# Kernel tuning notes

Measured on AMD Instinct MI355X. Metric: run time of the kernel, lower is better.

Reference implementation:

```python
import jax, jax.numpy as jnp
import numpy as np


def _ln(x, w, b, eps=1e-5):
    m = x.mean(-1, keepdims=True)
    v = ((x - m) ** 2).mean(-1, keepdims=True)
    return (x - m) * jax.lax.rsqrt(v + eps) * w + b


def _selective_scan(u, delta, A, Bm, Cm, D):
    # u, delta: (G, Dd, L); A: (G, Dd, N); Bm, Cm: (G, N, L); D: (G, Dd)
    G, Dd, L = u.shape
    N = A.shape[-1]

    def step(h, t):
        dt, ut, bt, ct = t  # (G,Dd), (G,Dd), (G,N), (G,N)
        h = jnp.exp(dt[..., None] * A) * h + (dt * ut)[..., None] * bt[:, None, :]
        return h, jnp.einsum('gdn,gn->gd', h, ct)

    h0 = jnp.zeros((G, Dd, N), u.dtype)
    xs_t = (jnp.moveaxis(delta, -1, 0), jnp.moveaxis(u, -1, 0),
            jnp.moveaxis(Bm, -1, 0), jnp.moveaxis(Cm, -1, 0))
    _, ys = jax.lax.scan(step, h0, xs_t)  # ys: (L, G, Dd)
    return jnp.moveaxis(ys, 0, -1) + D[..., None] * u


def _forward_core(xc, x_proj_w, dt_proj_w, dt_proj_b, A_log, Ds):
    # xc: (B, Di, H, W) -> SS2D 4-direction cross-scan selective scan
    B, Di, H, W = xc.shape
    L = H * W
    K, Ctot, _ = x_proj_w.shape
    N = A_log.shape[-1]
    R = Ctot - 2 * N
    x_hw = xc.reshape(B, Di, L)
    x_wh = xc.transpose(0, 1, 3, 2).reshape(B, Di, L)
    xs = jnp.stack([x_hw, x_wh, x_hw[:, :, ::-1], x_wh[:, :, ::-1]], axis=1)  # (B,K,Di,L)
    x_dbl = jnp.einsum('bkdl,kcd->bkcl', xs, x_proj_w)
    dtr, Bm, Cm = x_dbl[:, :, :R], x_dbl[:, :, R:R + N], x_dbl[:, :, R + N:]
    dts = jax.nn.softplus(jnp.einsum('bkrl,kdr->bkdl', dtr, dt_proj_w)
                          + dt_proj_b[None, :, :, None])
    A = -jnp.exp(A_log)  # (K, Di, N)
    G = B * K
    ys = _selective_scan(
        xs.reshape(G, Di, L), dts.reshape(G, Di, L),
        jnp.broadcast_to(A, (B, K, Di, N)).reshape(G, Di, N),
        Bm.reshape(G, N, L), Cm.reshape(G, N, L),
        jnp.broadcast_to(Ds, (B, K, Di)).reshape(G, Di),
    ).reshape(B, K, Di, L)
    inv_wh = lambda t: t.reshape(B, Di, W, H).transpose(0, 1, 3, 2).reshape(B, Di, L)
    y = ys[:, 0] + inv_wh(ys[:, 1]) + ys[:, 2, :, ::-1] + inv_wh(ys[:, 3, :, ::-1])
    return y.reshape(B, Di, H, W).transpose(0, 2, 3, 1)  # (B, H, W, Di)


def _vss_block(xh, ln_w, ln_b, in_w, cw, cb, xp, dtw, dtb, Alog, Dsk, onw, onb, ow):
    # xh: (B, H, W, C); residual VSS block with SS2D
    Di = cw.shape[0]
    h = _ln(xh, ln_w, ln_b)
    xz = h @ in_w.T  # (B,H,W,2*Di)
    xc, z = xz[..., :Di], xz[..., Di:]
    xc = xc.transpose(0, 3, 1, 2)  # (B,Di,H,W)
    xc = jax.lax.conv_general_dilated(
        xc, cw[:, None], (1, 1), 'SAME',
        feature_group_count=Di, dimension_numbers=('NCHW', 'OIHW', 'NCHW')
    ) + cb[None, :, None, None]
    xc = jax.nn.silu(xc)
    y = _forward_core(xc, xp, dtw, dtb, Alog, Dsk)
    y = _ln(y, onw, onb) * jax.nn.silu(z)
    return xh + y @ ow.T


def _fwd(x, skip, pe_expand_w, pe_norm_w, pe_norm_b, lp_w, lp_b,
         blk_ln_w, blk_ln_b, in_proj_w, conv_w, conv_b, x_proj_w,
         dt_proj_w, dt_proj_b, A_log, Ds, out_norm_w, out_norm_b, out_proj_w):
    B, Cin, H, W = x.shape
    c = Cin // 2
    xh = x.transpose(0, 2, 3, 1) @ pe_expand_w.T  # (B,H,W,2*Cin)
    xh = xh.reshape(B, H, W, 2, 2, c).transpose(0, 1, 3, 2, 4, 5).reshape(B, 2 * H, 2 * W, c)
    xh = _ln(xh, pe_norm_w, pe_norm_b)
    # concat with skip along channels, then per-pixel linear projection
    xh = jnp.concatenate([xh, skip.transpose(0, 2, 3, 1)], axis=-1)
    xh = xh @ lp_w.T + lp_b
    for i in range(blk_ln_w.shape[0]):
        xh = _vss_block(xh, blk_ln_w[i], blk_ln_b[i], in_proj_w[i], conv_w[i], conv_b[i],
                        x_proj_w[i], dt_proj_w[i], dt_proj_b[i], A_log[i], Ds[i],
                        out_norm_w[i], out_norm_b[i], out_proj_w[i])
    return xh.transpose(0, 3, 1, 2)  # (B, out_dim, 2H, 2W)


def setup_inputs():
    key = jax.random.key(0)
    ks = jax.random.split(key, 10)
    B, H, W = 2, 16, 16
    in_dim, skip_dim, out_dim, depth = 768, 384, 384, 2
    Di, N, R, K = 2 * out_dim, 16, out_dim // 16, 4
    s = 0.02
    return {
        'x': jax.random.normal(ks[0], (B, in_dim, H, W), jnp.float32),
        'skip': jax.random.normal(ks[1], (B, skip_dim, 2 * H, 2 * W), jnp.float32),
        'pe_expand_w': jax.random.normal(ks[2], (2 * in_dim, in_dim)) * s,
        'pe_norm_w': jnp.ones((in_dim // 2,)),
        'pe_norm_b': jnp.zeros((in_dim // 2,)),
        'lp_w': jax.random.normal(ks[3], (out_dim, skip_dim + in_dim // 2)) * s,
        'lp_b': jnp.zeros((out_dim,)),
        'blk_ln_w': jnp.ones((depth, out_dim)),
        'blk_ln_b': jnp.zeros((depth, out_dim)),
        'in_proj_w': jax.random.normal(ks[4], (depth, 2 * Di, out_dim)) * s,
        'conv_w': jax.random.normal(ks[5], (depth, Di, 3, 3)) * s,
        'conv_b': jnp.zeros((depth, Di)),
        'x_proj_w': jax.random.normal(ks[6], (depth, K, R + 2 * N, Di)) * s,
        'dt_proj_w': jax.random.normal(ks[7], (depth, K, Di, R)) * s,
        'dt_proj_b': jax.random.normal(ks[8], (depth, K, Di)) * s,
        'A_log': jnp.log(jnp.broadcast_to(jnp.arange(1, N + 1, dtype=jnp.float32), (depth, K, Di, N)) + 0.0),
        'Ds': jnp.ones((depth, K, Di)),
        'out_norm_w': jnp.ones((depth, Di)),
        'out_norm_b': jnp.zeros((depth, Di)),
        'out_proj_w': jax.random.normal(ks[9], (depth, out_dim, Di)) * s,
    }


def reference(x, skip, pe_expand_w, pe_norm_w, pe_norm_b, lp_w, lp_b,
              blk_ln_w, blk_ln_b, in_proj_w, conv_w, conv_b, x_proj_w,
              dt_proj_w, dt_proj_b, A_log, Ds, out_norm_w, out_norm_b, out_proj_w):
    return _fwd(x, skip, pe_expand_w, pe_norm_w, pe_norm_b, lp_w, lp_b,
                blk_ln_w, blk_ln_b, in_proj_w, conv_w, conv_b, x_proj_w,
                dt_proj_w, dt_proj_b, A_log, Ds, out_norm_w, out_norm_b, out_proj_w)
```

## Files before the change

### kernel.cpp

```cpp
#include <hip/hip_runtime.h>
#include <math.h>


typedef __attribute__((ext_vector_type(8))) short s8v;
typedef __attribute__((ext_vector_type(4))) float f4v;

static __device__ __forceinline__ float sigmoidf_(float x) {
    return 1.f / (1.f + __expf(-x));
}
static __device__ __forceinline__ ushort f2bf(float x) {
    unsigned u = __float_as_uint(x);
    return (ushort)((u + 0x7fff + ((u >> 16) & 1)) >> 16);
}
static __device__ __forceinline__ float bf2f(ushort u) {
    return __uint_as_float(((unsigned)u) << 16);
}

static __device__ __forceinline__ int scan_pos(int k, int l) {
    int m = (k & 2) ? (1023 - l) : l;
    return (k & 1) ? (((m & 31) << 5) | (m >> 5)) : m;
}

__global__ __launch_bounds__(256) void cvt_all_k(
    const float* __restrict__ pew, const float* __restrict__ lpw,
    const float* __restrict__ inw, const float* __restrict__ ow,
    const float* __restrict__ xpw, const float* __restrict__ dtw,
    ushort* __restrict__ wpe, ushort* __restrict__ wlp,
    ushort* __restrict__ winb, ushort* __restrict__ wob,
    ushort* __restrict__ wxpp, ushort* __restrict__ wdtp) {
    int g = blockIdx.x * 256 + threadIdx.x;
    if (g < 811008) {
        const float* s; ushort* d; int off;
        if (g < 294912)      { s = pew;  d = wpe;  off = g; }
        else if (g < 368640) { s = lpw;  d = wlp;  off = g - 294912; }
        else if (g < 663552) { s = inw;  d = winb; off = g - 368640; }
        else                 { s = ow;   d = wob;  off = g - 663552; }
        float4 v = ((const float4*)s)[off];
        ushort4 o = {f2bf(v.x), f2bf(v.y), f2bf(v.z), f2bf(v.w)};
        ((ushort4*)d)[off] = o;
    } else if (g < 909312) {
        int e = g - 811008;
        int blkb = e / 49152, rem = e % 49152;
        int n = rem / 192, q = rem % 192;
        int k = n >> 6, c = n & 63;
        ushort4 o = {0, 0, 0, 0};
        if (c < 56) {
            float4 v = *(const float4*)(xpw +
                ((size_t)((blkb * 4 + k) * 56 + c)) * 768 + q * 4);
            o = {f2bf(v.x), f2bf(v.y), f2bf(v.z), f2bf(v.w)};
        }
        ((ushort4*)wxpp)[e] = o;
    } else {
        int e = g - 909312;
        int rowk = e >> 3, q = e & 7;
        ushort4 o = {0, 0, 0, 0};
        if (q < 6) {
            float4 v = *(const float4*)(dtw + (size_t)rowk * 24 + q * 4);
            o = {f2bf(v.x), f2bf(v.y), f2bf(v.z), f2bf(v.w)};
        }
        ((ushort4*)wdtp)[e] = o;
    }
}

__global__ __launch_bounds__(256) void tr_x_k(const float* __restrict__ x,
                                              ushort* __restrict__ o) {
    __shared__ float tile[32][33];
    int b = blockIdx.z, c0 = blockIdx.y * 32, s0 = blockIdx.x * 32;
    int tx = threadIdx.x & 31, ty = threadIdx.x >> 5;
    for (int i = ty; i < 32; i += 8)
        tile[i][tx] = x[((size_t)(b * 768 + c0 + i)) * 256 + s0 + tx];
    __syncthreads();
    for (int i = ty; i < 32; i += 8)
        o[((size_t)(b * 256 + s0 + i)) * 768 + c0 + tx] = f2bf(tile[tx][i]);
}

__global__ __launch_bounds__(256) void peskip_k(const float* __restrict__ t1,
                                                const float* __restrict__ pnw,
                                                const float* __restrict__ pnb,
                                                const float* __restrict__ skip,
                                                ushort* __restrict__ cin) {
    __shared__ float tile[32][33];
    int bx = blockIdx.x;
    if (bx < 512) {
        int w = threadIdx.x >> 6, lane = threadIdx.x & 63;
        int row = bx * 4 + w;
        int b = row >> 10, p = row & 1023;
        int r = p >> 5, col = p & 31;
        int i = r >> 1, a = r & 1, j = col >> 1, b2 = col & 1;
        const float* src =
            t1 + ((size_t)(b * 256 + i * 16 + j)) * 1536 + (a * 2 + b2) * 384;
        float v[6], s1 = 0.f, s2 = 0.f;
#pragma unroll
        for (int q = 0; q < 6; ++q) {
            v[q] = src[lane + 64 * q];
            s1 += v[q]; s2 += v[q] * v[q];
        }
#pragma unroll
        for (int m = 1; m < 64; m <<= 1) {
            s1 += __shfl_xor(s1, m); s2 += __shfl_xor(s2, m);
        }
        float mean = s1 * (1.f / 384.f);
        float rstd = rsqrtf(s2 * (1.f / 384.f) - mean * mean + 1e-5f);
        ushort* o = cin + (size_t)row * 768;
#pragma unroll
        for (int q = 0; q < 6; ++q) {
            int c = lane + 64 * q;
            o[c] = f2bf((v[q] - mean) * rstd * pnw[c] + pnb[c]);
        }
    } else {
        int idx = bx - 512;
        int b = idx / 384, rem = idx % 384;
        int c0 = (rem / 32) * 32, s0 = (rem % 32) * 32;
        int tx = threadIdx.x & 31, ty = threadIdx.x >> 5;
        for (int i = ty; i < 32; i += 8)
            tile[i][tx] = skip[((size_t)(b * 384 + c0 + i)) * 1024 + s0 + tx];
        __syncthreads();
        for (int i = ty; i < 32; i += 8)
            cin[((size_t)(b * 1024 + s0 + i)) * 768 + 384 + c0 + tx] =
                f2bf(tile[tx][i]);
    }
}

__global__ __launch_bounds__(256) void tr_out_k(const float* __restrict__ xh,
                                                float* __restrict__ out) {
    __shared__ float tile[32][33];
    int b = blockIdx.z, p0 = blockIdx.x * 32, c0 = blockIdx.y * 32;
    int tx = threadIdx.x & 31, ty = threadIdx.x >> 5;
    for (int i = ty; i < 32; i += 8)
        tile[i][tx] = xh[((size_t)(b * 1024 + p0 + i)) * 384 + c0 + tx];
    __syncthreads();
    for (int i = ty; i < 32; i += 8)
        out[((size_t)(b * 384 + c0 + i)) * 1024 + p0 + tx] = tile[tx][i];
}

template <int BN>
__global__ __launch_bounds__(256) void gemm_t(const ushort* __restrict__ A,
                                              const ushort* __restrict__ B,
                                              const float* __restrict__ bias,
                                              const float* __restrict__ res,
                                              float* __restrict__ Cf,
                                              ushort* __restrict__ Cb,
                                              float* __restrict__ dblBC,
                                              ushort* __restrict__ dtrb,
                                              int M, int N, int K,
                                              long sAz, long sBz, long sBiz,
                                              long sCz, int mode) {
    constexpr int MI = (BN == 128) ? 4 : 2;
    __shared__ ushort Als[2][128][40];
    __shared__ ushort Bls[2][BN][40];
    A += (size_t)blockIdx.z * sAz;
    B += (size_t)blockIdx.z * sBz;
    if (Cf) Cf += (size_t)blockIdx.z * sCz;
    if (Cb) Cb += (size_t)blockIdx.z * sCz;
    if (bias) bias += (size_t)blockIdx.z * sBiz;
    int t = threadIdx.x;
    int bm = blockIdx.y * 128, bn = blockIdx.x * BN;
    int lane = t & 63, w = t >> 6;
    int wm = (BN == 128) ? (w & 1) * 64 : w * 32;
    int wn = (BN == 128) ? (w >> 1) * 64 : 0;
    int r16 = lane & 15, quad = lane >> 4;
    int srow = t >> 1, shalf = t & 1;
    int brow = (BN == 128) ? (t >> 1) : (t >> 2);
    int bq   = (BN == 128) ? (t & 1) * 16 : (t & 3) * 8;
    f4v acc[MI][4] = {};
    const ushort* Ag = A + (size_t)(bm + srow) * K + shalf * 16;
    const ushort* Bg = B + (size_t)(bn + brow) * K + bq;
    int nt = K >> 5;
    uint4 a0, a1, b0, b1;
    a0 = *(const uint4*)(Ag);
    a1 = *(const uint4*)(Ag + 8);
    b0 = *(const uint4*)(Bg);
    if (BN == 128) b1 = *(const uint4*)(Bg + 8);
    *(uint4*)&Als[0][srow][shalf * 16] = a0;
    *(uint4*)&Als[0][srow][shalf * 16 + 8] = a1;
    *(uint4*)&Bls[0][brow][bq] = b0;
    if (BN == 128) *(uint4*)&Bls[0][brow][bq + 8] = b1;
    for (int it = 0; it < nt; ++it) {
        int buf = it & 1;
        __syncthreads();
        if (it + 1 < nt) {
            int k0 = (it + 1) << 5;
            a0 = *(const uint4*)(Ag + k0);
            a1 = *(const uint4*)(Ag + k0 + 8);
            b0 = *(const uint4*)(Bg + k0);
            if (BN == 128) b1 = *(const uint4*)(Bg + k0 + 8);
        }
        s8v af[MI], bfr[4];
#pragma unroll
        for (int i = 0; i < MI; ++i)
            af[i] = *(const s8v*)&Als[buf][wm + i * 16 + r16][quad * 8];
#pragma unroll
        for (int j = 0; j < 4; ++j)
            bfr[j] = *(const s8v*)&Bls[buf][wn + j * 16 + r16][quad * 8];
#pragma unroll
        for (int i = 0; i < MI; ++i)
#pragma unroll
            for (int j = 0; j < 4; ++j)
                acc[i][j] = __builtin_amdgcn_mfma_f32_16x16x32_bf16(
                    af[i], bfr[j], acc[i][j], 0, 0, 0);
        if (it + 1 < nt) {
            *(uint4*)&Als[buf ^ 1][srow][shalf * 16] = a0;
            *(uint4*)&Als[buf ^ 1][srow][shalf * 16 + 8] = a1;
            *(uint4*)&Bls[buf ^ 1][brow][bq] = b0;
            if (BN == 128) *(uint4*)&Bls[buf ^ 1][brow][bq + 8] = b1;
        }
    }
#pragma unroll
    for (int i = 0; i < MI; ++i) {
        int row0 = bm + wm + i * 16 + quad * 4;
#pragma unroll
        for (int j = 0; j < 4; ++j) {
            int col = bn + wn + j * 16 + r16;
            float bv = bias ? bias[col] : 0.f;
#pragma unroll
            for (int r = 0; r < 4; ++r) {
                int row = row0 + r;
                float v = acc[i][j][r] + bv;
                if (mode == 0) {
                    if (res) v += res[(size_t)row * N + col];
                    Cf[(size_t)row * N + col] = v;
                } else if (mode == 1) {
                    v = (v > 20.f) ? v : __logf(1.f + __expf(v));
                    Cb[(size_t)row * N + col] = f2bf(v);
                } else {
                    int k = col >> 6, c = col & 63;
                    int b = row >> 10, p = row & 1023;
                    if (c < 32)
                        dtrb[((size_t)k * 2048 + row) * 32 + c] =
                            f2bf((c < 24) ? v : 0.f);
                    if (c >= 24 && c < 56) {
                        int l = scan_pos(k, p);
                        dblBC[(((size_t)(b * 4 + k)) * 1024 + l) * 32 + (c - 24)] = v;
                    }
                }
            }
        }
    }
}

__global__ __launch_bounds__(256) void dt_perm_k(const ushort* __restrict__ dtsp,
                                                 ushort* __restrict__ dtscan) {
    int r = blockIdx.x * 2 + (threadIdx.x >> 7);
    int t = threadIdx.x & 127;
    int l = r & 1023;
    int kb2 = r >> 10;
    int k = kb2 >> 1, b = kb2 & 1;
    int p = scan_pos(k, l);
    const uint* s = (const uint*)(dtsp + ((size_t)(k * 2048 + b * 1024 + p)) * 768);
    uint* d = (uint*)(dtscan + (size_t)r * 768);
    d[t] = s[t];
    d[t + 128] = s[t + 128];
    d[t + 256] = s[t + 256];
}

__global__ __launch_bounds__(256) void ln_rows_384(const float* __restrict__ in,
                                                   const float* __restrict__ wgt,
                                                   const float* __restrict__ bb,
                                                   ushort* __restrict__ out) {
    int w = threadIdx.x >> 6, lane = threadIdx.x & 63;
    int row = blockIdx.x * 4 + w;
    const float* x = in + (size_t)row * 384;
    float v[6], s1 = 0.f, s2 = 0.f;
#pragma unroll
    for (int q = 0; q < 6; ++q) {
        v[q] = x[lane + 64 * q];
        s1 += v[q]; s2 += v[q] * v[q];
    }
#pragma unroll
    for (int m = 1; m < 64; m <<= 1) {
        s1 += __shfl_xor(s1, m); s2 += __shfl_xor(s2, m);
    }
    float mean = s1 * (1.f / 384.f);
    float rstd = rsqrtf(s2 * (1.f / 384.f) - mean * mean + 1e-5f);
#pragma unroll
    for (int q = 0; q < 6; ++q) {
        int c = lane + 64 * q;
        out[(size_t)row * 384 + c] = f2bf((v[q] - mean) * rstd * wgt[c] + bb[c]);
    }
}

__global__ __launch_bounds__(256) void conv_silu_k(const float* __restrict__ xz,
                                                   const float* __restrict__ cw,
                                                   const float* __restrict__ cb,
                                                   ushort* __restrict__ xcb,
                                                   ushort* __restrict__ xcwh) {
    int row = blockIdx.x;
    int b = row >> 10, p = row & 1023;
    int r = p >> 5, col = p & 31;
    int mwh = ((p & 31) << 5) | (p >> 5);
    for (int d = threadIdx.x; d < 768; d += 256) {
        float acc = cb[d];
#pragma unroll
        for (int dy = 0; dy < 3; ++dy) {
            int rr = r + dy - 1;
            if ((unsigned)rr > 31u) continue;
#pragma unroll
            for (int dx = 0; dx < 3; ++dx) {
                int cc = col + dx - 1;
                if ((unsigned)cc > 31u) continue;
                acc += cw[d * 9 + dy * 3 + dx] *
                       xz[((size_t)(b * 1024 + rr * 32 + cc)) * 1536 + d];
            }
        }
        float o = acc * sigmoidf_(acc);
        ushort ob = f2bf(o);
        xcb[(size_t)row * 768 + d] = ob;
        xcwh[((size_t)(b * 1024 + mwh)) * 768 + d] = ob;
    }
}


__global__ __launch_bounds__(64) void scan_p1(const ushort* __restrict__ dtscan,
                                              const float* __restrict__ dblBC,
                                              const ushort* __restrict__ xcb,
                                              const ushort* __restrict__ xcwh,
                                              const float* __restrict__ alog,
                                              float* __restrict__ Pg,
                                              float* __restrict__ Hg) {
    __shared__ float sB[32][16];
    int lane = threadIdx.x;
    int d0 = blockIdx.x * 64, ch = blockIdx.y, kb = blockIdx.z;
    int k = kb & 3, b = kb >> 2;
    int d = d0 + lane;
    float A2[16];
    {
        const float4* ap = (const float4*)(alog + ((size_t)(k * 768 + d)) * 16);
#pragma unroll
        for (int q = 0; q < 4; ++q) {
            float4 v = ap[q];
            A2[4 * q + 0] = -__expf(v.x) * 1.44269504f;
            A2[4 * q + 1] = -__expf(v.y) * 1.44269504f;
            A2[4 * q + 2] = -__expf(v.z) * 1.44269504f;
            A2[4 * q + 3] = -__expf(v.w) * 1.44269504f;
        }
    }
    int l0 = ch * 32;
    const ushort* dts = dtscan + ((size_t)((k * 2 + b) * 1024 + l0)) * 768 + d;
    const ushort* ub = ((k & 1) ? xcwh : xcb) + (size_t)b * 786432 + d;
    const float* bcp = dblBC + (size_t)kb * 1024 * 32;
    float rdt[32], ru[32], rB[8];
#pragma unroll
    for (int i = 0; i < 32; ++i) rdt[i] = bf2f(dts[(size_t)i * 768]);
    if (k & 2) {
#pragma unroll
        for (int i = 0; i < 32; ++i)
            ru[i] = bf2f(ub[(size_t)(1023 - (l0 + i)) * 768]);
    } else {
#pragma unroll
        for (int i = 0; i < 32; ++i) ru[i] = bf2f(ub[(size_t)(l0 + i) * 768]);
    }
    int bi = lane >> 4, bn_ = lane & 15;
#pragma unroll
    for (int j = 0; j < 8; ++j)
        rB[j] = bcp[(size_t)(l0 + bi + 4 * j) * 32 + bn_];
#pragma unroll
    for (int j = 0; j < 8; ++j) sB[bi + 4 * j][bn_] = rB[j];
    __syncthreads();
    float h[16], P[16];
#pragma unroll
    for (int n = 0; n < 16; ++n) { h[n] = 0.f; P[n] = 1.f; }
#pragma unroll 4
    for (int i = 0; i < 32; ++i) {
        float dtv = rdt[i], dtu = dtv * ru[i];
        const float4* B4 = (const float4*)&sB[i][0];
        float4 q0 = B4[0], q1 = B4[1], q2 = B4[2], q3 = B4[3];
        float Bv[16] = {q0.x, q0.y, q0.z, q0.w, q1.x, q1.y, q1.z, q1.w,
                        q2.x, q2.y, q2.z, q2.w, q3.x, q3.y, q3.z, q3.w};
#pragma unroll
        for (int n = 0; n < 16; ++n) {
            float a = __builtin_amdgcn_exp2f(dtv * A2[n]);
            P[n] *= a;
            h[n] = a * h[n] + dtu * Bv[n];
        }
    }
    float* pp = Pg + ((size_t)(kb * 32 + ch)) * 12288 + d * 16;
    float* hp = Hg + ((size_t)(kb * 32 + ch)) * 12288 + d * 16;
#pragma unroll
    for (int q = 0; q < 4; ++q) {
        float4 pv = {P[4 * q], P[4 * q + 1], P[4 * q + 2], P[4 * q + 3]};
        float4 hv = {h[4 * q], h[4 * q + 1], h[4 * q + 2], h[4 * q + 3]};
        *(float4*)(pp + 4 * q) = pv;
        *(float4*)(hp + 4 * q) = hv;
    }
}

__global__ __launch_bounds__(256) void comb_k(const float* __restrict__ Pg,
                                              const float* __restrict__ Hg,
                                              float* __restrict__ H0g) {
    int t = blockIdx.x * 256 + threadIdx.x;
    int kb = t / 12288, dn = t % 12288;
    size_t base = (size_t)kb * 32 * 12288 + dn;
    float pv[31], hv[31];
#pragma unroll
    for (int ch = 0; ch < 31; ++ch) {
        pv[ch] = Pg[base + (size_t)ch * 12288];
        hv[ch] = Hg[base + (size_t)ch * 12288];
    }
    float h = 0.f;
    H0g[base] = 0.f;
#pragma unroll
    for (int ch = 0; ch < 31; ++ch) {
        h = pv[ch] * h + hv[ch];
        H0g[base + (size_t)(ch + 1) * 12288] = h;
    }
}

__global__ __launch_bounds__(64) void scan_p2(const ushort* __restrict__ dtscan,
                                              const float* __restrict__ dblBC,
                                              const ushort* __restrict__ xcb,
                                              const ushort* __restrict__ xcwh,
                                              const float* __restrict__ alog,
                                              const float* __restrict__ H0g,
                                              ushort* __restrict__ y4b) {
    __shared__ float sB[32][16];
    __shared__ float sC[32][16];
    int lane = threadIdx.x;
    int d0 = blockIdx.x * 64, ch = blockIdx.y, kb = blockIdx.z;
    int k = kb & 3, b = kb >> 2;
    int d = d0 + lane;
    float A2[16];
    {
        const float4* ap = (const float4*)(alog + ((size_t)(k * 768 + d)) * 16);
#pragma unroll
        for (int q = 0; q < 4; ++q) {
            float4 v = ap[q];
            A2[4 * q + 0] = -__expf(v.x) * 1.44269504f;
            A2[4 * q + 1] = -__expf(v.y) * 1.44269504f;
            A2[4 * q + 2] = -__expf(v.z) * 1.44269504f;
            A2[4 * q + 3] = -__expf(v.w) * 1.44269504f;
        }
    }
    float h[16];
    {
        const float4* h0p =
            (const float4*)(H0g + ((size_t)(kb * 32 + ch)) * 12288 + d * 16);
#pragma unroll
        for (int q = 0; q < 4; ++q) {
            float4 hv = h0p[q];
            h[4 * q + 0] = hv.x; h[4 * q + 1] = hv.y;
            h[4 * q + 2] = hv.z; h[4 * q + 3] = hv.w;
        }
    }
    int l0 = ch * 32;
    const ushort* dts = dtscan + ((size_t)((k * 2 + b) * 1024 + l0)) * 768 + d;
    const ushort* ub = ((k & 1) ? xcwh : xcb) + (size_t)b * 786432 + d;
    const float* bcp = dblBC + (size_t)kb * 1024 * 32;
    ushort* yp = y4b + ((size_t)(kb * 1024 + l0)) * 768 + d;
    float rdt[32], ru[32], rB[8], rC[8];
#pragma unroll
    for (int i = 0; i < 32; ++i) rdt[i] = bf2f(dts[(size_t)i * 768]);
    if (k & 2) {
#pragma unroll
        for (int i = 0; i < 32; ++i)
            ru[i] = bf2f(ub[(size_t)(1023 - (l0 + i)) * 768]);
    } else {
#pragma unroll
        for (int i = 0; i < 32; ++i) ru[i] = bf2f(ub[(size_t)(l0 + i) * 768]);
    }
    int bi = lane >> 4, bn_ = lane & 15;
#pragma unroll
    for (int j = 0; j < 8; ++j) {
        rB[j] = bcp[(size_t)(l0 + bi + 4 * j) * 32 + bn_];
        rC[j] = bcp[(size_t)(l0 + bi + 4 * j) * 32 + 16 + bn_];
    }
#pragma unroll
    for (int j = 0; j < 8; ++j) {
        sB[bi + 4 * j][bn_] = rB[j];
        sC[bi + 4 * j][bn_] = rC[j];
    }
    __syncthreads();
#pragma unroll 4
    for (int i = 0; i < 32; ++i) {
        float dtv = rdt[i], dtu = dtv * ru[i];
        const float4* B4 = (const float4*)&sB[i][0];
        const float4* C4 = (const float4*)&sC[i][0];
        float4 q0 = B4[0], q1 = B4[1], q2 = B4[2], q3 = B4[3];
        float Bv[16] = {q0.x, q0.y, q0.z, q0.w, q1.x, q1.y, q1.z, q1.w,
                        q2.x, q2.y, q2.z, q2.w, q3.x, q3.y, q3.z, q3.w};
        float4 c0 = C4[0], c1 = C4[1], c2 = C4[2], c3 = C4[3];
        float Cv[16] = {c0.x, c0.y, c0.z, c0.w, c1.x, c1.y, c1.z, c1.w,
                        c2.x, c2.y, c2.z, c2.w, c3.x, c3.y, c3.z, c3.w};
        float y = 0.f;
#pragma unroll
        for (int n = 0; n < 16; ++n) {
            float a = __builtin_amdgcn_exp2f(dtv * A2[n]);
            h[n] = a * h[n] + dtu * Bv[n];
            y += h[n] * Cv[n];
        }
        yp[(size_t)i * 768] = f2bf(y);
    }
}

__global__ __launch_bounds__(256) void fuse_out_k(const ushort* __restrict__ y4b,
                                                  const ushort* __restrict__ xcb,
                                                  const float* __restrict__ xz,
                                                  const float* __restrict__ ds,
                                                  const float* __restrict__ onw,
                                                  const float* __restrict__ onb,
                                                  ushort* __restrict__ g) {
    int w = threadIdx.x >> 6, lane = threadIdx.x & 63;
    int row = blockIdx.x * 4 + w;
    int b = row >> 10, p = row & 1023;
    int l0 = scan_pos(0, p), l1 = scan_pos(1, p);
    int l2 = scan_pos(2, p), l3 = scan_pos(3, p);
    const ushort* y0 = y4b + ((size_t)((b * 4 + 0) * 1024 + l0)) * 768;
    const ushort* y1 = y4b + ((size_t)((b * 4 + 1) * 1024 + l1)) * 768;
    const ushort* y2 = y4b + ((size_t)((b * 4 + 2) * 1024 + l2)) * 768;
    const ushort* y3 = y4b + ((size_t)((b * 4 + 3) * 1024 + l3)) * 768;
    float v[12], s1 = 0.f, s2 = 0.f;
#pragma unroll
    for (int q = 0; q < 12; ++q) {
        int d = lane + 64 * q;
        float u = bf2f(xcb[(size_t)row * 768 + d]);
        float dsum = ds[d] + ds[768 + d] + ds[1536 + d] + ds[2304 + d];
        float val = dsum * u + bf2f(y0[d]) + bf2f(y1[d]) + bf2f(y2[d]) + bf2f(y3[d]);
        v[q] = val; s1 += val; s2 += val * val;
    }
#pragma unroll
    for (int m = 1; m < 64; m <<= 1) {
        s1 += __shfl_xor(s1, m); s2 += __shfl_xor(s2, m);
    }
    float mean = s1 * (1.f / 768.f);
    float rstd = rsqrtf(s2 * (1.f / 768.f) - mean * mean + 1e-5f);
#pragma unroll
    for (int q = 0; q < 12; ++q) {
        int d = lane + 64 * q;
        float zz = xz[(size_t)row * 1536 + 768 + d];
        float sil = zz * sigmoidf_(zz);
        g[(size_t)row * 768 + d] = f2bf(((v[q] - mean) * rstd * onw[d] + onb[d]) * sil);
    }
}

extern "C" void kernel_launch(void* const* d_in, const int* in_sizes, int n_in,
                              void* d_out, int out_size, void* d_ws, size_t ws_size,
                              hipStream_t stream) {
    const float* x    = (const float*)d_in[0];
    const float* skip = (const float*)d_in[1];
    const float* pew  = (const float*)d_in[2];
    const float* pnw  = (const float*)d_in[3];
    const float* pnb  = (const float*)d_in[4];
    const float* lpw  = (const float*)d_in[5];
    const float* lpb  = (const float*)d_in[6];
    const float* blw  = (const float*)d_in[7];
    const float* blb  = (const float*)d_in[8];
    const float* inw  = (const float*)d_in[9];
    const float* cw   = (const float*)d_in[10];
    const float* cb   = (const float*)d_in[11];
    const float* xpw  = (const float*)d_in[12];
    const float* dtw  = (const float*)d_in[13];
    const float* dtbi = (const float*)d_in[14];
    const float* alog = (const float*)d_in[15];
    const float* ds   = (const float*)d_in[16];
    const float* onw  = (const float*)d_in[17];
    const float* onb  = (const float*)d_in[18];
    const float* ow   = (const float*)d_in[19];
    float* out = (float*)d_out;

    char* base = (char*)d_ws;
    auto alloc = [&](size_t bytes) -> char* {
        char* p = base;
        base += (bytes + 255) & ~(size_t)255;
        return p;
    };
    float*  xh    = (float*)alloc(2048 * 384 * 4);
    ushort* hbuf  = (ushort*)alloc(2048 * 768 * 2);
    float*  xz    = (float*)alloc((size_t)2048 * 1536 * 4);
    ushort* xcb   = (ushort*)alloc(2048 * 768 * 2);
    ushort* xcwh  = (ushort*)alloc(2048 * 768 * 2);
    float*  dblBC = (float*)alloc(8192 * 32 * 4);
    ushort* dtrb  = (ushort*)alloc((size_t)4 * 2048 * 32 * 2);
    ushort* dtsp  = (ushort*)alloc((size_t)4 * 2048 * 768 * 2);
    ushort* dtscan= (ushort*)alloc((size_t)4 * 2048 * 768 * 2);
    ushort* y4b   = (ushort*)alloc((size_t)8192 * 768 * 2);
    float*  Pg    = (float*)alloc((size_t)8 * 32 * 12288 * 4);
    float*  Hg    = (float*)alloc((size_t)8 * 32 * 12288 * 4);
    float*  H0g   = (float*)alloc((size_t)8 * 32 * 12288 * 4);
    ushort* xspe  = (ushort*)alloc(512 * 768 * 2);
    float*  t1    = (float*)alloc(512 * 1536 * 4);
    ushort* wpe   = (ushort*)alloc((size_t)1536 * 768 * 2);
    ushort* wlp   = (ushort*)alloc(384 * 768 * 2);
    ushort* winb  = (ushort*)alloc((size_t)2 * 1536 * 384 * 2);
    ushort* wob   = (ushort*)alloc((size_t)2 * 384 * 768 * 2);
    ushort* wxpp  = (ushort*)alloc((size_t)2 * 256 * 768 * 2);
    ushort* wdtp  = (ushort*)alloc((size_t)2 * 4 * 768 * 32 * 2);

    cvt_all_k<<<3744, 256, 0, stream>>>(pew, lpw, inw, ow, xpw, dtw,
                                        wpe, wlp, winb, wob, wxpp, wdtp);

    tr_x_k<<<dim3(8, 24, 2), 256, 0, stream>>>(x, xspe);
    gemm_t<64><<<dim3(24, 4), 256, 0, stream>>>(xspe, wpe, nullptr, nullptr, t1,
                                                nullptr, nullptr, nullptr,
                                                512, 1536, 768, 0, 0, 0, 0, 0);
    peskip_k<<<1280, 256, 0, stream>>>(t1, pnw, pnb, skip, hbuf);
    gemm_t<64><<<dim3(6, 16), 256, 0, stream>>>(hbuf, wlp, lpb, nullptr, xh,
                                                nullptr, nullptr, nullptr,
                                                2048, 384, 768, 0, 0, 0, 0, 0);

    for (int blk = 0; blk < 2; ++blk) {
        const ushort* inw_i = winb + (size_t)blk * 1536 * 384;
        const float*  cw_i  = cw + (size_t)blk * 768 * 9;
        const float*  cb_i  = cb + (size_t)blk * 768;
        const ushort* xpw_i = wxpp + (size_t)blk * 256 * 768;
        const ushort* dtw_i = wdtp + (size_t)blk * 4 * 768 * 32;
        const float*  dtb_i = dtbi + (size_t)blk * 4 * 768;
        const float*  al_i  = alog + (size_t)blk * 4 * 768 * 16;
        const float*  ds_i  = ds + (size_t)blk * 4 * 768;
        const float*  onw_i = onw + (size_t)blk * 768;
        const float*  onb_i = onb + (size_t)blk * 768;
        const ushort* ow_i  = wob + (size_t)blk * 384 * 768;

        ln_rows_384<<<512, 256, 0, stream>>>(xh, blw + blk * 384, blb + blk * 384,
                                             hbuf);
        gemm_t<128><<<dim3(12, 16), 256, 0, stream>>>(hbuf, inw_i, nullptr,
                                                      nullptr, xz, nullptr,
                                                      nullptr, nullptr,
                                                      2048, 1536, 384,
                                                      0, 0, 0, 0, 0);
        conv_silu_k<<<2048, 256, 0, stream>>>(xz, cw_i, cb_i, xcb, xcwh);
        gemm_t<64><<<dim3(4, 16), 256, 0, stream>>>(xcb, xpw_i, nullptr, nullptr,
                                                    nullptr, nullptr, dblBC, dtrb,
                                                    2048, 256, 768, 0, 0, 0, 0, 2);
        gemm_t<128><<<dim3(6, 16, 4), 256, 0, stream>>>(dtrb, dtw_i, dtb_i,
                                                        nullptr, nullptr, dtsp,
                                                        nullptr, nullptr,
                                                        2048, 768, 32,
                                                        2048 * 32, 768 * 32, 768,
                                                        (long)2048 * 768, 1);
        dt_perm_k<<<4096, 256, 0, stream>>>(dtsp, dtscan);
        scan_p1<<<dim3(12, 31, 8), 64, 0, stream>>>(dtscan, dblBC, xcb, xcwh,
                                                    al_i, Pg, Hg);
        comb_k<<<384, 256, 0, stream>>>(Pg, Hg, H0g);
        scan_p2<<<dim3(12, 32, 8), 64, 0, stream>>>(dtscan, dblBC, xcb, xcwh,
                                                    al_i, H0g, y4b);
        fuse_out_k<<<512, 256, 0, stream>>>(y4b, xcb, xz, ds_i, onw_i, onb_i,
                                            hbuf);
        gemm_t<64><<<dim3(6, 16), 256, 0, stream>>>(hbuf, ow_i, nullptr, xh, xh,
                                                    nullptr, nullptr, nullptr,
                                                    2048, 384, 768, 0, 0, 0, 0, 0);
    }

    tr_out_k<<<dim3(32, 12, 2), 256, 0, stream>>>(xh, out);
}
```

Measured before the change: 464.6 us.

## Use 64x64 GEMM tiles everywhere and store in_proj output as bf16

Replaces the templated 128-row GEMM with one 64x64-tile kernel where each of four waves computes a 32x32 quadrant, doubling or more the grid sizes for better CU occupancy on these small GEMMs. Adds a mode that writes the in_proj output as bf16, and the conv and output-gate kernels now read that bf16 buffer instead of fp32. This halves the traffic of the large xz intermediate and raises parallelism, at the cost of less data reuse per tile and lower precision for the conv input and z gate. An empty leftover loop was left in the epilogue.

```diff
diff --git a/kernel.cpp b/kernel.cpp
--- a/kernel.cpp
+++ b/kernel.cpp
@@ -133,8 +133,7 @@
         out[((size_t)(b * 384 + c0 + i)) * 1024 + p0 + tx] = tile[tx][i];
 }
 
-template <int BN>
-__global__ __launch_bounds__(256) void gemm_t(const ushort* __restrict__ A,
+__global__ __launch_bounds__(256) void gemm64(const ushort* __restrict__ A,
                                               const ushort* __restrict__ B,
                                               const float* __restrict__ bias,
                                               const float* __restrict__ res,
@@ -145,73 +144,63 @@
                                               int M, int N, int K,
                                               long sAz, long sBz, long sBiz,
                                               long sCz, int mode) {
-    constexpr int MI = (BN == 128) ? 4 : 2;
-    __shared__ ushort Als[2][128][40];
-    __shared__ ushort Bls[2][BN][40];
+    __shared__ ushort Als[2][64][40];
+    __shared__ ushort Bls[2][64][40];
     A += (size_t)blockIdx.z * sAz;
     B += (size_t)blockIdx.z * sBz;
     if (Cf) Cf += (size_t)blockIdx.z * sCz;
     if (Cb) Cb += (size_t)blockIdx.z * sCz;
     if (bias) bias += (size_t)blockIdx.z * sBiz;
     int t = threadIdx.x;
-    int bm = blockIdx.y * 128, bn = blockIdx.x * BN;
+    int bm = blockIdx.y * 64, bn = blockIdx.x * 64;
     int lane = t & 63, w = t >> 6;
-    int wm = (BN == 128) ? (w & 1) * 64 : w * 32;
-    int wn = (BN == 128) ? (w >> 1) * 64 : 0;
+    int wm = (w & 1) * 32, wn = (w >> 1) * 32;
     int r16 = lane & 15, quad = lane >> 4;
-    int srow = t >> 1, shalf = t & 1;
-    int brow = (BN == 128) ? (t >> 1) : (t >> 2);
-    int bq   = (BN == 128) ? (t & 1) * 16 : (t & 3) * 8;
-    f4v acc[MI][4] = {};
-    const ushort* Ag = A + (size_t)(bm + srow) * K + shalf * 16;
-    const ushort* Bg = B + (size_t)(bn + brow) * K + bq;
+    int srow = t >> 2, sq = (t & 3) * 8;
+    f4v acc[2][2] = {};
+    const ushort* Ag = A + (size_t)(bm + srow) * K + sq;
+    const ushort* Bg = B + (size_t)(bn + srow) * K + sq;
     int nt = K >> 5;
-    uint4 a0, a1, b0, b1;
-    a0 = *(const uint4*)(Ag);
-    a1 = *(const uint4*)(Ag + 8);
-    b0 = *(const uint4*)(Bg);
-    if (BN == 128) b1 = *(const uint4*)(Bg + 8);
-    *(uint4*)&Als[0][srow][shalf * 16] = a0;
-    *(uint4*)&Als[0][srow][shalf * 16 + 8] = a1;
-    *(uint4*)&Bls[0][brow][bq] = b0;
-    if (BN == 128) *(uint4*)&Bls[0][brow][bq + 8] = b1;
+    uint4 a0 = *(const uint4*)(Ag);
+    uint4 b0 = *(const uint4*)(Bg);
+    *(uint4*)&Als[0][srow][sq] = a0;
+    *(uint4*)&Bls[0][srow][sq] = b0;
     for (int it = 0; it < nt; ++it) {
         int buf = it & 1;
         __syncthreads();
         if (it + 1 < nt) {
             int k0 = (it + 1) << 5;
             a0 = *(const uint4*)(Ag + k0);
-            a1 = *(const uint4*)(Ag + k0 + 8);
             b0 = *(const uint4*)(Bg + k0);
-            if (BN == 128) b1 = *(const uint4*)(Bg + k0 + 8);
-        }
-        s8v af[MI], bfr[4];
-#pragma unroll
-        for (int i = 0; i < MI; ++i)
+        }
+        s8v af[2], bfr[2];
+#pragma unroll
+        for (int i = 0; i < 2; ++i)
             af[i] = *(const s8v*)&Als[buf][wm + i * 16 + r16][quad * 8];
 #pragma unroll
-        for (int j = 0; j < 4; ++j)
+        for (int j = 0; j < 2; ++j)
             bfr[j] = *(const s8v*)&Bls[buf][wn + j * 16 + r16][quad * 8];
 #pragma unroll
-        for (int i = 0; i < MI; ++i)
-#pragma unroll
-            for (int j = 0; j < 4; ++j)
+        for (int i = 0; i < 2; ++i)
+#pragma unroll
+            for (int j = 0; j < 2; ++j)
                 acc[i][j] = __builtin_amdgcn_mfma_f32_16x16x32_bf16(
                     af[i], bfr[j], acc[i][j], 0, 0, 0);
         if (it + 1 < nt) {
-            *(uint4*)&Als[buf ^ 1][srow][shalf * 16] = a0;
-            *(uint4*)&Als[buf ^ 1][srow][shalf * 16 + 8] = a1;
-            *(uint4*)&Bls[buf ^ 1][brow][bq] = b0;
-            if (BN == 128) *(uint4*)&Bls[buf ^ 1][brow][bq + 8] = b1;
-        }
-    }
-#pragma unroll
-    for (int i = 0; i < MI; ++i) {
+            *(uint4*)&Als[buf ^ 1][srow][sq] = a0;
+            *(uint4*)&Bls[buf ^ 1][srow][sq] = b0;
+        }
+    }
+#pragma unroll
+    for (int i = 0; i < 2; ++i) {
         int row0 = bm + wm + i * 16 + quad * 4;
 #pragma unroll
-        for (int j = 0; j < 4; ++j) {
+        for (int j = 0; j < 2; ++j) {
             int col = bn + wn + j * 16 + r16;
             float bv = bias ? bias[col] : 0.f;
+#pragma unroll
+            for (int r = 0; r < 2 * 2; ++r) {
+            }
 #pragma unroll
             for (int r = 0; r < 4; ++r) {
                 int row = row0 + r;
@@ -221,6 +210,8 @@
                     Cf[(size_t)row * N + col] = v;
                 } else if (mode == 1) {
                     v = (v > 20.f) ? v : __logf(1.f + __expf(v));
+                    Cb[(size_t)row * N + col] = f2bf(v);
+                } else if (mode == 3) {
                     Cb[(size_t)row * N + col] = f2bf(v);
                 } else {
                     int k = col >> 6, c = col & 63;
@@ -279,7 +270,7 @@
     }
 }
 
-__global__ __launch_bounds__(256) void conv_silu_k(const float* __restrict__ xz,
+__global__ __launch_bounds__(256) void conv_silu_k(const ushort* __restrict__ xzb,
                                                    const float* __restrict__ cw,
                                                    const float* __restrict__ cb,
                                                    ushort* __restrict__ xcb,
@@ -299,7 +290,7 @@
                 int cc = col + dx - 1;
                 if ((unsigned)cc > 31u) continue;
                 acc += cw[d * 9 + dy * 3 + dx] *
-                       xz[((size_t)(b * 1024 + rr * 32 + cc)) * 1536 + d];
+                       bf2f(xzb[((size_t)(b * 1024 + rr * 32 + cc)) * 1536 + d]);
             }
         }
         float o = acc * sigmoidf_(acc);
@@ -493,7 +484,7 @@
 
 __global__ __launch_bounds__(256) void fuse_out_k(const ushort* __restrict__ y4b,
                                                   const ushort* __restrict__ xcb,
-                                                  const float* __restrict__ xz,
+                                                  const ushort* __restrict__ xzb,
                                                   const float* __restrict__ ds,
                                                   const float* __restrict__ onw,
                                                   const float* __restrict__ onb,
@@ -525,7 +516,7 @@
 #pragma unroll
     for (int q = 0; q < 12; ++q) {
         int d = lane + 64 * q;
-        float zz = xz[(size_t)row * 1536 + 768 + d];
+        float zz = bf2f(xzb[(size_t)row * 1536 + 768 + d]);
         float sil = zz * sigmoidf_(zz);
         g[(size_t)row * 768 + d] = f2bf(((v[q] - mean) * rstd * onw[d] + onb[d]) * sil);
     }
@@ -564,7 +555,7 @@
     };
     float*  xh    = (float*)alloc(2048 * 384 * 4);
     ushort* hbuf  = (ushort*)alloc(2048 * 768 * 2);
-    float*  xz    = (float*)alloc((size_t)2048 * 1536 * 4);
+    ushort* xzb   = (ushort*)alloc((size_t)2048 * 1536 * 2);
     ushort* xcb   = (ushort*)alloc(2048 * 768 * 2);
     ushort* xcwh  = (ushort*)alloc(2048 * 768 * 2);
     float*  dblBC = (float*)alloc(8192 * 32 * 4);
@@ -588,13 +579,13 @@
                                         wpe, wlp, winb, wob, wxpp, wdtp);
 
     tr_x_k<<<dim3(8, 24, 2), 256, 0, stream>>>(x, xspe);
-    gemm_t<64><<<dim3(24, 4), 256, 0, stream>>>(xspe, wpe, nullptr, nullptr, t1,
-                                                nullptr, nullptr, nullptr,
-                                                512, 1536, 768, 0, 0, 0, 0, 0);
+    gemm64<<<dim3(24, 8), 256, 0, stream>>>(xspe, wpe, nullptr, nullptr, t1,
+                                            nullptr, nullptr, nullptr,
+                                            512, 1536, 768, 0, 0, 0, 0, 0);
     peskip_k<<<1280, 256, 0, stream>>>(t1, pnw, pnb, skip, hbuf);
-    gemm_t<64><<<dim3(6, 16), 256, 0, stream>>>(hbuf, wlp, lpb, nullptr, xh,
-                                                nullptr, nullptr, nullptr,
-                                                2048, 384, 768, 0, 0, 0, 0, 0);
+    gemm64<<<dim3(6, 32), 256, 0, stream>>>(hbuf, wlp, lpb, nullptr, xh,
+                                            nullptr, nullptr, nullptr,
+                                            2048, 384, 768, 0, 0, 0, 0, 0);
 
     for (int blk = 0; blk < 2; ++blk) {
         const ushort* inw_i = winb + (size_t)blk * 1536 * 384;
@@ -611,32 +602,29 @@
 
         ln_rows_384<<<512, 256, 0, stream>>>(xh, blw + blk * 384, blb + blk * 384,
                                              hbuf);
-        gemm_t<128><<<dim3(12, 16), 256, 0, stream>>>(hbuf, inw_i, nullptr,
-                                                      nullptr, xz, nullptr,
-                                                      nullptr, nullptr,
-                                                      2048, 1536, 384,
-                                                      0, 0, 0, 0, 0);
-        conv_silu_k<<<2048, 256, 0, stream>>>(xz, cw_i, cb_i, xcb, xcwh);
-        gemm_t<64><<<dim3(4, 16), 256, 0, stream>>>(xcb, xpw_i, nullptr, nullptr,
-                                                    nullptr, nullptr, dblBC, dtrb,
-                                                    2048, 256, 768, 0, 0, 0, 0, 2);
-        gemm_t<128><<<dim3(6, 16, 4), 256, 0, stream>>>(dtrb, dtw_i, dtb_i,
-                                                        nullptr, nullptr, dtsp,
-                                                        nullptr, nullptr,
-                                                        2048, 768, 32,
-                                                        2048 * 32, 768 * 32, 768,
-                                                        (long)2048 * 768, 1);
+        gemm64<<<dim3(24, 32), 256, 0, stream>>>(hbuf, inw_i, nullptr, nullptr,
+                                                 nullptr, xzb, nullptr, nullptr,
+                                                 2048, 1536, 384, 0, 0, 0, 0, 3);
+        conv_silu_k<<<2048, 256, 0, stream>>>(xzb, cw_i, cb_i, xcb, xcwh);
+        gemm64<<<dim3(4, 32), 256, 0, stream>>>(xcb, xpw_i, nullptr, nullptr,
+                                                nullptr, nullptr, dblBC, dtrb,
+                                                2048, 256, 768, 0, 0, 0, 0, 2);
+        gemm64<<<dim3(12, 32, 4), 256, 0, stream>>>(dtrb, dtw_i, dtb_i, nullptr,
+                                                    nullptr, dtsp, nullptr, nullptr,
+                                                    2048, 768, 32,
+                                                    2048 * 32, 768 * 32, 768,
+                                                    (long)2048 * 768, 1);
         dt_perm_k<<<4096, 256, 0, stream>>>(dtsp, dtscan);
         scan_p1<<<dim3(12, 31, 8), 64, 0, stream>>>(dtscan, dblBC, xcb, xcwh,
                                                     al_i, Pg, Hg);
         comb_k<<<384, 256, 0, stream>>>(Pg, Hg, H0g);
         scan_p2<<<dim3(12, 32, 8), 64, 0, stream>>>(dtscan, dblBC, xcb, xcwh,
                                                     al_i, H0g, y4b);
-        fuse_out_k<<<512, 256, 0, stream>>>(y4b, xcb, xz, ds_i, onw_i, onb_i,
+        fuse_out_k<<<512, 256, 0, stream>>>(y4b, xcb, xzb, ds_i, onw_i, onb_i,
                                             hbuf);
-        gemm_t<64><<<dim3(6, 16), 256, 0, stream>>>(hbuf, ow_i, nullptr, xh, xh,
-                                                    nullptr, nullptr, nullptr,
-                                                    2048, 384, 768, 0, 0, 0, 0, 0);
+        gemm64<<<dim3(6, 32), 256, 0, stream>>>(hbuf, ow_i, nullptr, xh, xh,
+                                                nullptr, nullptr, nullptr,
+                                                2048, 384, 768, 0, 0, 0, 0, 0);
     }
 
     tr_out_k<<<dim3(32, 12, 2), 256, 0, stream>>>(xh, out);
```

After: 404.7 us. -12.9%, faster.
